# Kernel tuning notes

Hardware: AMD Instinct MI355X
Metric: run time of the kernel (lower is better)

## Reference

```python
import jax, jax.numpy as jnp
import numpy as np

B, N, C = 2, 2048, 1024
H = 16
D = C // H  # head_dim = 64
SCALE = D ** -0.5


def setup_inputs() -> dict:
    key = jax.random.key(0)
    k1, k2, k3, k4 = jax.random.split(key, 4)
    x = jax.random.normal(k1, (B, N, C), dtype=jnp.float32)
    # nn.Linear(in_dim, 3*out_dim, bias=False): store as [in, 3*out] for x @ W
    w_qkv = jax.random.normal(k2, (C, 3 * C), dtype=jnp.float32) * (C ** -0.5)
    w_proj = jax.random.normal(k3, (C, C), dtype=jnp.float32) * (C ** -0.5)
    b_proj = jax.random.normal(k4, (C,), dtype=jnp.float32) * 0.01
    return {"x": x, "w_qkv": w_qkv, "w_proj": w_proj, "b_proj": b_proj}


def reference(x, w_qkv, w_proj, b_proj):
    b, n, c = x.shape
    # QKV projection -> [3, B, H, N, D]
    qkv = (x @ w_qkv).reshape(b, n, 3, H, D).transpose(2, 0, 3, 1, 4)
    q, k, v = qkv[0], qkv[1], qkv[2]
    # scaled dot-product attention, full [B, H, N, N] scores as in original
    attn = jax.nn.softmax(jnp.einsum('bhqd,bhkd->bhqk', q * SCALE, k), axis=-1)
    out = jnp.einsum('bhqk,bhkd->bhqd', attn, v)  # [B, H, N, D]
    out = out.transpose(0, 2, 1, 3).reshape(b, n, c)
    return out @ w_proj + b_proj
```

## Files before the change

kernel.cpp:

```cpp
#include <hip/hip_runtime.h>

typedef unsigned short u16;
typedef float f32x4 __attribute__((ext_vector_type(4)));
typedef short bf16x8 __attribute__((ext_vector_type(8)));
typedef u16 u16x4 __attribute__((ext_vector_type(4)));
typedef u16 u16x8 __attribute__((ext_vector_type(8)));
typedef __bf16 bfr4 __attribute__((ext_vector_type(4)));

#define BB 2
#define NN 2048
#define CC 1024
#define HH 16
#define DD 64
#define MM (BB * NN)
#define NQKV (3 * CC)
#define QSCALE 0.18033688011112042f

#if __has_builtin(__builtin_amdgcn_exp2f)
#define EXP2(x) __builtin_amdgcn_exp2f(x)
#else
#define EXP2(x) exp2f(x)
#endif

__device__ __forceinline__ u16 f2bf(float f) {
    unsigned u = __float_as_uint(f);
    u += 0x7FFFu + ((u >> 16) & 1u);
    return (u16)(u >> 16);
}

__device__ __forceinline__ void ld_lds16(const u16* g, u16* l) {
    __builtin_amdgcn_global_load_lds(
        (const __attribute__((address_space(1))) unsigned int*)g,
        (__attribute__((address_space(3))) unsigned int*)l, 16, 0, 0);
}

__global__ __launch_bounds__(256) void k_prep(const float* __restrict__ x,
                                              const float* __restrict__ wqkv,
                                              const float* __restrict__ wproj,
                                              u16* __restrict__ Xb,
                                              u16* __restrict__ Wq,
                                              u16* __restrict__ Wp) {
    __shared__ float tile[32][33];
    int bid = blockIdx.x, t = threadIdx.x;
    if (bid < 2048) {
        int i = (bid * 256 + t) * 8;
        float4 a = *(const float4*)(x + i);
        float4 b = *(const float4*)(x + i + 4);
        u16x8 o;
        o[0] = f2bf(a.x); o[1] = f2bf(a.y); o[2] = f2bf(a.z); o[3] = f2bf(a.w);
        o[4] = f2bf(b.x); o[5] = f2bf(b.y); o[6] = f2bf(b.z); o[7] = f2bf(b.w);
        *(u16x8*)(Xb + i) = o;
        return;
    }
    const float* in;
    u16* out;
    int Nn, n0, k0;
    if (bid < 2048 + 3072) {
        int b2 = bid - 2048;
        in = wqkv; out = Wq; Nn = NQKV;
        n0 = (b2 % 96) * 32; k0 = (b2 / 96) * 32;
    } else {
        int b3 = bid - 5120;
        in = wproj; out = Wp; Nn = CC;
        n0 = (b3 & 31) * 32; k0 = (b3 >> 5) * 32;
    }
    int tx = t & 31, ty = t >> 5;
#pragma unroll
    for (int r = 0; r < 32; r += 8)
        tile[ty + r][tx] = in[(size_t)(k0 + ty + r) * Nn + n0 + tx];
    __syncthreads();
#pragma unroll
    for (int r = 0; r < 32; r += 8)
        out[(size_t)(n0 + ty + r) * CC + k0 + tx] = f2bf(tile[tx][ty + r]);
}

__global__ __launch_bounds__(512, 2) void k_gemmq(
    const u16* __restrict__ A, const u16* __restrict__ B,
    u16* __restrict__ Qb, u16* __restrict__ Kb, u16* __restrict__ Vb) {
    const int Kd = 1024;
    __shared__ __align__(16) u16 Ah0[256][64], Bh0[192][64];
    __shared__ __align__(16) u16 Ah1[256][64], Bh1[192][64];

    int t = threadIdx.x, wave = t >> 6, lane = t & 63;
    int quad = lane >> 4, l16 = lane & 15;
    int wr = wave >> 2, wc = wave & 3;

    int cid = blockIdx.y * 16 + blockIdx.x;
    int swz = (cid & 7) * 32 + (cid >> 3);
    int m0 = (swz >> 4) * 256, n0 = (swz & 15) * 192;

    int strow = wave * 8 + (lane >> 3);
    int stdst = (lane & 7) * 8;
    int stsrc = ((lane & 7) ^ (lane >> 3)) * 8;

    f32x4 acc[8][3];
#pragma unroll
    for (int i = 0; i < 8; i++)
#pragma unroll
        for (int j = 0; j < 3; j++) acc[i][j] = f32x4{0.f, 0.f, 0.f, 0.f};

    auto STAGE = [&](int k0, u16 (*Ad)[64], u16 (*Bd)[64]) {
#pragma unroll
        for (int i = 0; i < 4; i++) {
            int row = i * 64 + strow;
            ld_lds16(A + (size_t)(m0 + row) * Kd + k0 + stsrc, &Ad[row][stdst]);
        }
#pragma unroll
        for (int i = 0; i < 3; i++) {
            int row = i * 64 + strow;
            ld_lds16(B + (size_t)(n0 + row) * Kd + k0 + stsrc, &Bd[row][stdst]);
        }
    };
    auto COMPUTE = [&](u16 (*As)[64], u16 (*Bs)[64]) {
#pragma unroll
        for (int s = 0; s < 2; s++) {
            int pos = ((s * 4 + quad) ^ (l16 & 7)) * 8;
            bf16x8 af[8], bg[3];
#pragma unroll
            for (int m = 0; m < 8; m++)
                af[m] = *(const bf16x8*)&As[wr * 128 + m * 16 + l16][pos];
#pragma unroll
            for (int n = 0; n < 3; n++)
                bg[n] = *(const bf16x8*)&Bs[wc * 48 + n * 16 + l16][pos];
            __builtin_amdgcn_s_setprio(1);
#pragma unroll
            for (int m = 0; m < 8; m++)
#pragma unroll
                for (int n = 0; n < 3; n++)
                    acc[m][n] = __builtin_amdgcn_mfma_f32_16x16x32_bf16(
                        af[m], bg[n], acc[m][n], 0, 0, 0);
            __builtin_amdgcn_s_setprio(0);
        }
    };

    STAGE(0, Ah0, Bh0);
    __syncthreads();
    for (int k0 = 0; k0 < Kd; k0 += 128) {
        STAGE(k0 + 64, Ah1, Bh1);
        COMPUTE(Ah0, Bh0);
        __syncthreads();
        if (k0 + 128 < Kd) STAGE(k0 + 128, Ah0, Bh0);
        COMPUTE(Ah1, Bh1);
        __syncthreads();
    }

#pragma unroll
    for (int m = 0; m < 8; m++)
#pragma unroll
        for (int n = 0; n < 3; n++)
#pragma unroll
            for (int r = 0; r < 4; r++) {
                int grow = m0 + wr * 128 + m * 16 + quad * 4 + r;
                int gcol = n0 + wc * 48 + n * 16 + l16;
                float v = acc[m][n][r];
                int three = gcol >> 10, rem = gcol & 1023;
                int h = rem >> 6, d = rem & 63;
                int bb = grow >> 11, nn = grow & 2047;
                if (three == 0) {
                    Qb[((size_t)(bb * HH + h) * NN + nn) * DD + d] = f2bf(v * QSCALE);
                } else if (three == 1) {
                    Kb[((size_t)(bb * HH + h) * NN + nn) * DD + d] = f2bf(v);
                } else {
                    Vb[((size_t)(bb * HH + h) * DD + d) * NN + nn] = f2bf(v);
                }
            }
}

__global__ __launch_bounds__(256) void k_gemmp(
    const u16* __restrict__ A, const u16* __restrict__ B,
    const float* __restrict__ bias, float* __restrict__ Cout) {
    const int Kd = 1024;
    __shared__ __align__(16) u16 Ah[64][128];
    __shared__ __align__(16) u16 Bh[128][128];

    int t = threadIdx.x, wave = t >> 6, lane = t & 63;
    int quad = lane >> 4, l16 = lane & 15;
    int m0 = blockIdx.x * 64, n0 = blockIdx.y * 128;

    int strow = lane >> 4;
    int stdst = (lane & 15) * 8;

    f32x4 acc[4][2];
#pragma unroll
    for (int i = 0; i < 4; i++)
#pragma unroll
        for (int j = 0; j < 2; j++) acc[i][j] = f32x4{0.f, 0.f, 0.f, 0.f};

    auto STAGE = [&](int k0) {
#pragma unroll
        for (int i = 0; i < 4; i++) {
            int row = wave * 16 + i * 4 + strow;
            int src = ((lane & 15) ^ (row & 7)) * 8;
            ld_lds16(A + (size_t)(m0 + row) * Kd + k0 + src, &Ah[row & 63][0] + stdst);
        }
#pragma unroll
        for (int i = 0; i < 8; i++) {
            int row = wave * 32 + i * 4 + strow;
            int src = ((lane & 15) ^ (row & 7)) * 8;
            ld_lds16(B + (size_t)(n0 + row) * Kd + k0 + src, &Bh[row & 127][0] + stdst);
        }
    };
    auto COMPUTE = [&]() {
#pragma unroll
        for (int s = 0; s < 4; s++) {
            int pos = ((s * 4 + quad) ^ (l16 & 7)) * 8;
            bf16x8 af[4], bg[2];
#pragma unroll
            for (int m = 0; m < 4; m++)
                af[m] = *(const bf16x8*)&Ah[m * 16 + l16][pos];
#pragma unroll
            for (int n = 0; n < 2; n++)
                bg[n] = *(const bf16x8*)&Bh[wave * 32 + n * 16 + l16][pos];
            __builtin_amdgcn_s_setprio(1);
#pragma unroll
            for (int m = 0; m < 4; m++)
#pragma unroll
                for (int n = 0; n < 2; n++)
                    acc[m][n] = __builtin_amdgcn_mfma_f32_16x16x32_bf16(
                        af[m], bg[n], acc[m][n], 0, 0, 0);
            __builtin_amdgcn_s_setprio(0);
        }
    };

    for (int k0 = 0; k0 < Kd; k0 += 128) {
        __syncthreads();
        STAGE(k0);
        __syncthreads();
        COMPUTE();
    }

#pragma unroll
    for (int m = 0; m < 4; m++)
#pragma unroll
        for (int n = 0; n < 2; n++)
#pragma unroll
            for (int r = 0; r < 4; r++) {
                int grow = m0 + m * 16 + quad * 4 + r;
                int gcol = n0 + wave * 32 + n * 16 + l16;
                Cout[(size_t)grow * CC + gcol] = acc[m][n][r] + bias[gcol];
            }
}

__global__ __launch_bounds__(512) void k_attn(const u16* __restrict__ Qb,
                                              const u16* __restrict__ Kb,
                                              const u16* __restrict__ VbT,
                                              u16* __restrict__ Ob) {
    __shared__ __align__(16) u16 Ks0[64][64], Ks1[64][64];
    __shared__ __align__(16) u16 Vs0[64][64], Vs1[64][64];
    __shared__ __align__(16) u16 Ps[8][16][72];

    int t = threadIdx.x, wave = t >> 6, lane = t & 63;
    int quad = lane >> 4, l16 = lane & 15;
    int bh = blockIdx.x, q0 = blockIdx.y * 128;
    const size_t kbase = (size_t)bh * NN * DD;
    const size_t vbase = (size_t)bh * DD * NN;

    int qrow = q0 + wave * 16 + l16;
    bf16x8 qf0 = *(const bf16x8*)&Qb[kbase + (size_t)qrow * DD + quad * 8];
    bf16x8 qf1 = *(const bf16x8*)&Qb[kbase + (size_t)qrow * DD + 32 + quad * 8];

    f32x4 o[4];
#pragma unroll
    for (int i = 0; i < 4; i++) o[i] = f32x4{0.f, 0.f, 0.f, 0.f};
    f32x4 lrow = f32x4{0.f, 0.f, 0.f, 0.f};

    int stgrp = lane & 7;
    int stsrc = (stgrp ^ (lane >> 3)) * 8;
    int strow = wave * 8 + (lane >> 3);
    int cf0 = (quad ^ (l16 & 7)) * 8;
    int cf1 = ((4 + quad) ^ (l16 & 7)) * 8;

    auto STAGE = [&](int cc, u16 (*Kd_)[64], u16 (*Vd_)[64]) {
        ld_lds16(&Kb[kbase + (size_t)(cc * 64 + strow) * DD + stsrc],
                 &Kd_[strow][stgrp * 8]);
        ld_lds16(&VbT[vbase + (size_t)strow * NN + cc * 64 + stsrc],
                 &Vd_[strow][stgrp * 8]);
    };

    auto COMPUTE = [&](u16 (*Ksrc)[64], u16 (*Vsrc)[64]) {
        bf16x8 kf[4][2];
#pragma unroll
        for (int kt = 0; kt < 4; kt++) {
            kf[kt][0] = *(const bf16x8*)&Ksrc[kt * 16 + l16][cf0];
            kf[kt][1] = *(const bf16x8*)&Ksrc[kt * 16 + l16][cf1];
        }
        f32x4 s[4];
        __builtin_amdgcn_s_setprio(1);
#pragma unroll
        for (int kt = 0; kt < 4; kt++) {
            f32x4 z = f32x4{0.f, 0.f, 0.f, 0.f};
            z = __builtin_amdgcn_mfma_f32_16x16x32_bf16(kf[kt][0], qf0, z, 0, 0, 0);
            z = __builtin_amdgcn_mfma_f32_16x16x32_bf16(kf[kt][1], qf1, z, 0, 0, 0);
            s[kt] = z;
        }
        __builtin_amdgcn_s_setprio(0);
#pragma unroll
        for (int kt = 0; kt < 4; kt++) {
            bfr4 pk;
#pragma unroll
            for (int r = 0; r < 4; r++) {
                float e = EXP2(s[kt][r]);
                lrow[r] += e;
                pk[r] = (__bf16)e;
            }
            *(bfr4*)&Ps[wave][l16][kt * 16 + quad * 4] = pk;
        }
        __asm__ volatile("s_waitcnt lgkmcnt(0)" ::: "memory");
        bf16x8 pb0 = *(const bf16x8*)&Ps[wave][l16][quad * 8];
        bf16x8 pb1 = *(const bf16x8*)&Ps[wave][l16][32 + quad * 8];
        __builtin_amdgcn_s_setprio(1);
#pragma unroll
        for (int dt = 0; dt < 4; dt++) {
            bf16x8 vf0 = *(const bf16x8*)&Vsrc[dt * 16 + l16][cf0];
            bf16x8 vf1 = *(const bf16x8*)&Vsrc[dt * 16 + l16][cf1];
            o[dt] = __builtin_amdgcn_mfma_f32_16x16x32_bf16(vf0, pb0, o[dt], 0, 0, 0);
            o[dt] = __builtin_amdgcn_mfma_f32_16x16x32_bf16(vf1, pb1, o[dt], 0, 0, 0);
        }
        __builtin_amdgcn_s_setprio(0);
    };

    STAGE(0, Ks0, Vs0);
    __syncthreads();

    for (int c = 0; c < NN / 64; c += 2) {
        STAGE(c + 1, Ks1, Vs1);
        COMPUTE(Ks0, Vs0);
        __syncthreads();
        if (c + 2 < NN / 64) STAGE(c + 2, Ks0, Vs0);
        COMPUTE(Ks1, Vs1);
        __syncthreads();
    }

    int b = bh >> 4, h = bh & 15;
    float l = (lrow[0] + lrow[1]) + (lrow[2] + lrow[3]);
    l += __shfl_xor(l, 16, 64);
    l += __shfl_xor(l, 32, 64);
    float inv = 1.f / l;
    int grow = b * NN + q0 + wave * 16 + l16;
#pragma unroll
    for (int dt = 0; dt < 4; dt++) {
        u16x4 hv;
#pragma unroll
        for (int r = 0; r < 4; r++) hv[r] = f2bf(o[dt][r] * inv);
        int gcol = h * DD + dt * 16 + quad * 4;
        *(u16x4*)&Ob[(size_t)grow * CC + gcol] = hv;
    }
}

extern "C" void kernel_launch(void* const* d_in, const int* in_sizes, int n_in,
                              void* d_out, int out_size, void* d_ws, size_t ws_size,
                              hipStream_t stream) {
    const float* x      = (const float*)d_in[0];
    const float* w_qkv  = (const float*)d_in[1];
    const float* w_proj = (const float*)d_in[2];
    const float* b_proj = (const float*)d_in[3];
    float* out = (float*)d_out;

    u16* p = (u16*)d_ws;
    u16* Xb = p; p += (size_t)MM * CC;
    u16* Wq = p; p += (size_t)NQKV * CC;
    u16* Wp = p; p += (size_t)CC * CC;
    u16* Qb = p; p += (size_t)MM * CC;
    u16* Kb = p; p += (size_t)MM * CC;
    u16* Vb = p; p += (size_t)MM * CC;
    u16* Ob = p; p += (size_t)MM * CC;

    k_prep<<<2048 + 3072 + 1024, 256, 0, stream>>>(x, w_qkv, w_proj, Xb, Wq, Wp);
    k_gemmq<<<dim3(NQKV / 192, MM / 256), 512, 0, stream>>>(Xb, Wq, Qb, Kb, Vb);
    k_attn<<<dim3(BB * HH, NN / 128), 512, 0, stream>>>(Qb, Kb, Vb, Ob);
    k_gemmp<<<dim3(MM / 64, CC / 128), 256, 0, stream>>>(Ob, Wp, b_proj, out);
}
```

Baseline: 184.3 us.

## Deepen QKV GEMM prefetch and load attention V fragments directly from global

The QKV GEMM now keeps two stages in flight, using explicit vmcnt waits and raw s_barrier instead of __syncthreads, so the next tile's loads overlap more compute. The attention kernel stops staging V through LDS, reading V^T fragments straight from global memory into registers, and stages K in 128-row chunks processed as two 64-key halves. This cuts LDS traffic and barrier count per key, at the cost of uncached global V loads with exposed latency and more register pressure. The hand-written vmcnt(7) count depends on the exact number of outstanding loads per STAGE.

```diff
diff --git a/kernel.cpp b/kernel.cpp
--- a/kernel.cpp
+++ b/kernel.cpp
@@ -21,6 +21,10 @@
 #else
 #define EXP2(x) exp2f(x)
 #endif
+
+#define BARRIER() __asm__ volatile("s_barrier" ::: "memory")
+#define WAITV7()  __asm__ volatile("s_waitcnt vmcnt(7)" ::: "memory")
+#define WAITV0()  __asm__ volatile("s_waitcnt vmcnt(0)" ::: "memory")
 
 __device__ __forceinline__ u16 f2bf(float f) {
     unsigned u = __float_as_uint(f);
@@ -134,14 +138,19 @@
     };
 
     STAGE(0, Ah0, Bh0);
-    __syncthreads();
+    STAGE(64, Ah1, Bh1);
+    WAITV7(); BARRIER();
     for (int k0 = 0; k0 < Kd; k0 += 128) {
-        STAGE(k0 + 64, Ah1, Bh1);
         COMPUTE(Ah0, Bh0);
-        __syncthreads();
-        if (k0 + 128 < Kd) STAGE(k0 + 128, Ah0, Bh0);
+        BARRIER();
+        if (k0 + 128 < Kd) { STAGE(k0 + 128, Ah0, Bh0); WAITV7(); }
+        else WAITV0();
+        BARRIER();
         COMPUTE(Ah1, Bh1);
-        __syncthreads();
+        BARRIER();
+        if (k0 + 192 < Kd) { STAGE(k0 + 192, Ah1, Bh1); WAITV7(); }
+        else WAITV0();
+        BARRIER();
     }
 
 #pragma unroll
@@ -245,8 +254,7 @@
                                               const u16* __restrict__ Kb,
                                               const u16* __restrict__ VbT,
                                               u16* __restrict__ Ob) {
-    __shared__ __align__(16) u16 Ks0[64][64], Ks1[64][64];
-    __shared__ __align__(16) u16 Vs0[64][64], Vs1[64][64];
+    __shared__ __align__(16) u16 Ks0[128][64], Ks1[128][64];
     __shared__ __align__(16) u16 Ps[8][16][72];
 
     int t = threadIdx.x, wave = t >> 6, lane = t & 63;
@@ -270,19 +278,29 @@
     int cf0 = (quad ^ (l16 & 7)) * 8;
     int cf1 = ((4 + quad) ^ (l16 & 7)) * 8;
 
-    auto STAGE = [&](int cc, u16 (*Kd_)[64], u16 (*Vd_)[64]) {
-        ld_lds16(&Kb[kbase + (size_t)(cc * 64 + strow) * DD + stsrc],
-                 &Kd_[strow][stgrp * 8]);
-        ld_lds16(&VbT[vbase + (size_t)strow * NN + cc * 64 + stsrc],
-                 &Vd_[strow][stgrp * 8]);
-    };
-
-    auto COMPUTE = [&](u16 (*Ksrc)[64], u16 (*Vsrc)[64]) {
+    auto STAGE = [&](int cc, u16 (*Kd_)[64]) {
+#pragma unroll
+        for (int ii = 0; ii < 2; ii++) {
+            int row = strow + ii * 64;
+            ld_lds16(&Kb[kbase + (size_t)(cc * 128 + row) * DD + stsrc],
+                     &Kd_[row][stgrp * 8]);
+        }
+    };
+
+    auto HALF = [&](int cc, int h, u16 (*Ksrc)[64]) {
+        bf16x8 vf[4][2];
+#pragma unroll
+        for (int dt = 0; dt < 4; dt++) {
+            const u16* vp = VbT + vbase + (size_t)(dt * 16 + l16) * NN
+                          + cc * 128 + h * 64;
+            vf[dt][0] = *(const bf16x8*)(vp + quad * 8);
+            vf[dt][1] = *(const bf16x8*)(vp + 32 + quad * 8);
+        }
         bf16x8 kf[4][2];
 #pragma unroll
         for (int kt = 0; kt < 4; kt++) {
-            kf[kt][0] = *(const bf16x8*)&Ksrc[kt * 16 + l16][cf0];
-            kf[kt][1] = *(const bf16x8*)&Ksrc[kt * 16 + l16][cf1];
+            kf[kt][0] = *(const bf16x8*)&Ksrc[h * 64 + kt * 16 + l16][cf0];
+            kf[kt][1] = *(const bf16x8*)&Ksrc[h * 64 + kt * 16 + l16][cf1];
         }
         f32x4 s[4];
         __builtin_amdgcn_s_setprio(1);
@@ -311,23 +329,23 @@
         __builtin_amdgcn_s_setprio(1);
 #pragma unroll
         for (int dt = 0; dt < 4; dt++) {
-            bf16x8 vf0 = *(const bf16x8*)&Vsrc[dt * 16 + l16][cf0];
-            bf16x8 vf1 = *(const bf16x8*)&Vsrc[dt * 16 + l16][cf1];
-            o[dt] = __builtin_amdgcn_mfma_f32_16x16x32_bf16(vf0, pb0, o[dt], 0, 0, 0);
-            o[dt] = __builtin_amdgcn_mfma_f32_16x16x32_bf16(vf1, pb1, o[dt], 0, 0, 0);
+            o[dt] = __builtin_amdgcn_mfma_f32_16x16x32_bf16(vf[dt][0], pb0, o[dt], 0, 0, 0);
+            o[dt] = __builtin_amdgcn_mfma_f32_16x16x32_bf16(vf[dt][1], pb1, o[dt], 0, 0, 0);
         }
         __builtin_amdgcn_s_setprio(0);
     };
 
-    STAGE(0, Ks0, Vs0);
+    STAGE(0, Ks0);
     __syncthreads();
 
-    for (int c = 0; c < NN / 64; c += 2) {
-        STAGE(c + 1, Ks1, Vs1);
-        COMPUTE(Ks0, Vs0);
+    for (int c = 0; c < NN / 128; c += 2) {
+        STAGE(c + 1, Ks1);
+        HALF(c, 0, Ks0);
+        HALF(c, 1, Ks0);
         __syncthreads();
-        if (c + 2 < NN / 64) STAGE(c + 2, Ks0, Vs0);
-        COMPUTE(Ks1, Vs1);
+        if (c + 2 < NN / 128) STAGE(c + 2, Ks0);
+        HALF(c + 1, 0, Ks1);
+        HALF(c + 1, 1, Ks1);
         __syncthreads();
     }
 
```

Measured after the change: 272.8 us. 1.48x slower.
